# Performance work log

Hardware: AMD Instinct MI355X
Metric: run time of the kernel (lower is better)

The kernel has to match this reference:

```python
import jax, jax.numpy as jnp
import numpy as np

NUM_CLASS = 1000
DIMS = 2048
NUM_HEADS = 8
HEAD = DIMS // NUM_HEADS  # 256
ALPHA = 0.999
N = 16384


def setup_inputs() -> dict:
    key = jax.random.key(0)
    k1, k2, k3 = jax.random.split(key, 3)
    x = jax.random.normal(k1, (N, DIMS), dtype=jnp.float32)
    labels = jax.random.randint(k2, (N,), 0, NUM_CLASS)
    centers = jax.random.normal(k3, (NUM_CLASS, NUM_HEADS, HEAD), dtype=jnp.float32)
    return {"x": x, "labels": labels, "centers": centers}


def reference(x, labels, centers):
    # gather per-sample centers: [N, H, hd]
    c = centers[labels]
    xh = x.reshape(-1, NUM_HEADS, HEAD)  # [N, H, hd]
    # per-head MSE, sum over heads, mean over batch
    loss = jnp.mean(jnp.square(xh - c), axis=-1).sum(axis=-1).mean()
    new_centers = centers.at[labels].set(ALPHA * c + (1.0 - ALPHA) * xh)
    return loss, new_centers
```

## Files before the change

### kernel.cpp

```cpp
#include <hip/hip_runtime.h>

#define NUM_CLASS 1000
#define DIMS 2048
#define NHEADS 8
#define HEAD (DIMS / NHEADS)
#define NBATCH 16384
#define ALPHA 0.999f

#define LOSS_SCALE (1.0f / (16384.0f * 256.0f))

__device__ __forceinline__ float wave_reduce_sum(float v) {
    #pragma unroll
    for (int off = 32; off > 0; off >>= 1)
        v += __shfl_down(v, off, 64);
    return v;
}

__global__ void last_idx_kernel(const int* __restrict__ labels, int* __restrict__ last) {
    int i = blockIdx.x * blockDim.x + threadIdx.x;
    if (i < NBATCH) {
        atomicMax(&last[labels[i]], i);
    }
}

__global__ void loss_kernel(const float* __restrict__ x,
                            const int* __restrict__ labels,
                            const float* __restrict__ centers,
                            float* __restrict__ out_loss) {
    const int total4 = NBATCH * (DIMS / 4);
    const int row4 = DIMS / 4;

    float acc = 0.0f;
    for (int i = blockIdx.x * blockDim.x + threadIdx.x; i < total4;
         i += gridDim.x * blockDim.x) {
        int row  = i >> 9;
        int col4 = i & (row4 - 1);
        int lbl  = labels[row];
        float4 xv = reinterpret_cast<const float4*>(x)[i];
        float4 cv = reinterpret_cast<const float4*>(centers)[lbl * row4 + col4];
        float dx = xv.x - cv.x;
        float dy = xv.y - cv.y;
        float dz = xv.z - cv.z;
        float dw = xv.w - cv.w;
        acc += dx * dx + dy * dy + dz * dz + dw * dw;
    }

    __shared__ float sm[4];
    int lane = threadIdx.x & 63;
    int wid  = threadIdx.x >> 6;
    acc = wave_reduce_sum(acc);
    if (lane == 0) sm[wid] = acc;
    __syncthreads();
    if (wid == 0) {
        float v = (lane < 4) ? sm[lane] : 0.0f;
        v = wave_reduce_sum(v);
        if (lane == 0) atomicAdd(out_loss, v * LOSS_SCALE);
    }
}

__global__ void update_kernel(const float* __restrict__ x,
                              const float* __restrict__ centers,
                              const int* __restrict__ last,
                              float* __restrict__ newc) {
    int i = blockIdx.x * blockDim.x + threadIdx.x;
    if (i >= NUM_CLASS * DIMS) return;
    int k = i >> 11;
    int d = i & (DIMS - 1);
    float c = centers[i];
    int li = last[k];
    float v = c;
    if (li >= 0) {
        float xv = x[li * DIMS + d];
        v = ALPHA * c + (1.0f - ALPHA) * xv;
    }
    newc[i] = v;
}

extern "C" void kernel_launch(void* const* d_in, const int* in_sizes, int n_in,
                              void* d_out, int out_size, void* d_ws, size_t ws_size,
                              hipStream_t stream) {
    const float* x       = (const float*)d_in[0];
    const int*   labels  = (const int*)d_in[1];
    const float* centers = (const float*)d_in[2];

    float* out_loss = (float*)d_out;
    float* out_newc = (float*)d_out + 1;

    int* last = (int*)d_ws;

    hipMemsetAsync(last, 0xFF, NUM_CLASS * sizeof(int), stream);
    hipMemsetAsync(out_loss, 0, sizeof(float), stream);

    last_idx_kernel<<<(NBATCH + 255) / 256, 256, 0, stream>>>(labels, last);

    loss_kernel<<<2048, 256, 0, stream>>>(x, labels, centers, out_loss);

    update_kernel<<<(NUM_CLASS * DIMS + 255) / 256, 256, 0, stream>>>(
        x, centers, last, out_newc);
}
```

Measured before the change: 232.7 us.

## Fuse last-index, loss and center update into one heterogeneous kernel

Replaces three kernels and a workspace memset with a single launch. The first 1000 blocks each scan all labels to find the last sample index for their class and write the EMA-updated center row. The remaining blocks compute the loss row by row with float4 loads. This removes launch overhead and the atomicMax pass, at the cost of every update block redundantly reading the whole label array. The output is at offset 1 float, so the float4 path is not used for stores, which are written as scalars.

```diff
diff --git a/kernel.cpp b/kernel.cpp
--- a/kernel.cpp
+++ b/kernel.cpp
@@ -2,78 +2,100 @@
 
 #define NUM_CLASS 1000
 #define DIMS 2048
-#define NHEADS 8
-#define HEAD (DIMS / NHEADS)
 #define NBATCH 16384
 #define ALPHA 0.999f
-
 #define LOSS_SCALE (1.0f / (16384.0f * 256.0f))
 
-__device__ __forceinline__ float wave_reduce_sum(float v) {
-    #pragma unroll
-    for (int off = 32; off > 0; off >>= 1)
-        v += __shfl_down(v, off, 64);
-    return v;
-}
+#define BLOCK 256
+#define LOSS_BLOCKS 3096
+#define TOTAL_BLOCKS (NUM_CLASS + LOSS_BLOCKS)
 
-__global__ void last_idx_kernel(const int* __restrict__ labels, int* __restrict__ last) {
-    int i = blockIdx.x * blockDim.x + threadIdx.x;
-    if (i < NBATCH) {
-        atomicMax(&last[labels[i]], i);
+__global__ __launch_bounds__(BLOCK) void fused_kernel(
+    const float* __restrict__ x,
+    const int* __restrict__ labels,
+    const float* __restrict__ centers,
+    float* __restrict__ out_loss,
+    float* __restrict__ newc) {
+    __shared__ float smf[4];
+    __shared__ int smi[4];
+    const int tid  = threadIdx.x;
+    const int lane = tid & 63;
+    const int wid  = tid >> 6;
+    const int b    = blockIdx.x;
+
+    if (b < NUM_CLASS) {
+        int best = -1;
+        for (int i = tid; i < NBATCH; i += BLOCK) {
+            if (labels[i] == b) best = i;
+        }
+        #pragma unroll
+        for (int off = 32; off > 0; off >>= 1) {
+            int o = __shfl_down(best, off, 64);
+            best = best > o ? best : o;
+        }
+        if (lane == 0) smi[wid] = best;
+        __syncthreads();
+        if (tid == 0) {
+            int v01 = smi[0] > smi[1] ? smi[0] : smi[1];
+            int v23 = smi[2] > smi[3] ? smi[2] : smi[3];
+            smi[0] = v01 > v23 ? v01 : v23;
+        }
+        __syncthreads();
+        const int li = smi[0];
+
+        const float4* crow = reinterpret_cast<const float4*>(centers + (size_t)b * DIMS);
+        float* orow = newc + (size_t)b * DIMS;
+        if (li >= 0) {
+            const float4* xrow = reinterpret_cast<const float4*>(x + (size_t)li * DIMS);
+            #pragma unroll
+            for (int j = 0; j < DIMS / 4 / BLOCK; ++j) {
+                int e = j * BLOCK + tid;
+                float4 c4 = crow[e];
+                float4 x4 = xrow[e];
+                float* o = orow + e * 4;
+                o[0] = ALPHA * c4.x + (1.0f - ALPHA) * x4.x;
+                o[1] = ALPHA * c4.y + (1.0f - ALPHA) * x4.y;
+                o[2] = ALPHA * c4.z + (1.0f - ALPHA) * x4.z;
+                o[3] = ALPHA * c4.w + (1.0f - ALPHA) * x4.w;
+            }
+        } else {
+            #pragma unroll
+            for (int j = 0; j < DIMS / 4 / BLOCK; ++j) {
+                int e = j * BLOCK + tid;
+                float4 c4 = crow[e];
+                float* o = orow + e * 4;
+                o[0] = c4.x; o[1] = c4.y; o[2] = c4.z; o[3] = c4.w;
+            }
+        }
+    } else {
+        const int lb = b - NUM_CLASS;
+        float acc = 0.0f;
+        for (int row = lb; row < NBATCH; row += LOSS_BLOCKS) {
+            const int label = labels[row];
+            const float4* xr = reinterpret_cast<const float4*>(x + (size_t)row * DIMS);
+            const float4* cr = reinterpret_cast<const float4*>(centers + (size_t)label * DIMS);
+            #pragma unroll
+            for (int j = 0; j < DIMS / 4 / BLOCK; ++j) {
+                int e = j * BLOCK + tid;
+                float4 xv = xr[e];
+                float4 cv = cr[e];
+                float dx = xv.x - cv.x;
+                float dy = xv.y - cv.y;
+                float dz = xv.z - cv.z;
+                float dw = xv.w - cv.w;
+                acc += dx * dx + dy * dy + dz * dz + dw * dw;
+            }
+        }
+        #pragma unroll
+        for (int off = 32; off > 0; off >>= 1)
+            acc += __shfl_down(acc, off, 64);
+        if (lane == 0) smf[wid] = acc;
+        __syncthreads();
+        if (tid == 0) {
+            float v = (smf[0] + smf[1]) + (smf[2] + smf[3]);
+            atomicAdd(out_loss, v * LOSS_SCALE);
+        }
     }
-}
-
-__global__ void loss_kernel(const float* __restrict__ x,
-                            const int* __restrict__ labels,
-                            const float* __restrict__ centers,
-                            float* __restrict__ out_loss) {
-    const int total4 = NBATCH * (DIMS / 4);
-    const int row4 = DIMS / 4;
-
-    float acc = 0.0f;
-    for (int i = blockIdx.x * blockDim.x + threadIdx.x; i < total4;
-         i += gridDim.x * blockDim.x) {
-        int row  = i >> 9;
-        int col4 = i & (row4 - 1);
-        int lbl  = labels[row];
-        float4 xv = reinterpret_cast<const float4*>(x)[i];
-        float4 cv = reinterpret_cast<const float4*>(centers)[lbl * row4 + col4];
-        float dx = xv.x - cv.x;
-        float dy = xv.y - cv.y;
-        float dz = xv.z - cv.z;
-        float dw = xv.w - cv.w;
-        acc += dx * dx + dy * dy + dz * dz + dw * dw;
-    }
-
-    __shared__ float sm[4];
-    int lane = threadIdx.x & 63;
-    int wid  = threadIdx.x >> 6;
-    acc = wave_reduce_sum(acc);
-    if (lane == 0) sm[wid] = acc;
-    __syncthreads();
-    if (wid == 0) {
-        float v = (lane < 4) ? sm[lane] : 0.0f;
-        v = wave_reduce_sum(v);
-        if (lane == 0) atomicAdd(out_loss, v * LOSS_SCALE);
-    }
-}
-
-__global__ void update_kernel(const float* __restrict__ x,
-                              const float* __restrict__ centers,
-                              const int* __restrict__ last,
-                              float* __restrict__ newc) {
-    int i = blockIdx.x * blockDim.x + threadIdx.x;
-    if (i >= NUM_CLASS * DIMS) return;
-    int k = i >> 11;
-    int d = i & (DIMS - 1);
-    float c = centers[i];
-    int li = last[k];
-    float v = c;
-    if (li >= 0) {
-        float xv = x[li * DIMS + d];
-        v = ALPHA * c + (1.0f - ALPHA) * xv;
-    }
-    newc[i] = v;
 }
 
 extern "C" void kernel_launch(void* const* d_in, const int* in_sizes, int n_in,
@@ -86,15 +108,7 @@
     float* out_loss = (float*)d_out;
     float* out_newc = (float*)d_out + 1;
 
-    int* last = (int*)d_ws;
-
-    hipMemsetAsync(last, 0xFF, NUM_CLASS * sizeof(int), stream);
     hipMemsetAsync(out_loss, 0, sizeof(float), stream);
-
-    last_idx_kernel<<<(NBATCH + 255) / 256, 256, 0, stream>>>(labels, last);
-
-    loss_kernel<<<2048, 256, 0, stream>>>(x, labels, centers, out_loss);
-
-    update_kernel<<<(NUM_CLASS * DIMS + 255) / 256, 256, 0, stream>>>(
-        x, centers, last, out_newc);
+    fused_kernel<<<TOTAL_BLOCKS, BLOCK, 0, stream>>>(x, labels, centers,
+                                                     out_loss, out_newc);
 }
```

New measurement: 215.3 us. 1.08x faster.
